# Kernel optimization log

Hardware: AMD Instinct MI355X
Metric: run time of the kernel (lower is better)

The kernel has to match this reference:

```python
import jax, jax.numpy as jnp
import numpy as np

ORDER = 5
LOOKAHEAD = 0
NDF = 96  # n_df_bins


def setup_inputs() -> dict:
    key = jax.random.key(0)
    k1, k2, k3 = jax.random.split(key, 3)
    spec = jax.random.normal(k1, (16, 1, 2000, 481, 2), dtype=jnp.float32)
    coefs = jax.random.normal(k2, (16, 2000, ORDER, NDF, 2), dtype=jnp.float32)
    alpha = jax.random.uniform(k3, (16, 2000, 1), dtype=jnp.float32)
    return {"spec": spec, "coefs": coefs, "alpha": alpha}


def reference(spec, coefs, alpha):
    # spec: [B, 1, T, F, 2]; coefs: [B, T, ORDER, NDF, 2]; alpha: [B, T, 1]
    B, _, T, F, _ = spec.shape
    x = spec[:, 0, :, :NDF, :]  # [B, T, NDF, 2]
    # pad time axis: (order - lookahead - 1) before, lookahead after
    xp = jnp.pad(x, ((0, 0), (ORDER - LOOKAHEAD - 1, LOOKAHEAD), (0, 0), (0, 0)))
    # overlapping time windows of length ORDER (loop over small fixed tap count)
    w = jnp.stack([xp[:, k:k + T] for k in range(ORDER)], axis=2)  # [B, T, ORDER, NDF, 2]
    # complex multiply-accumulate per tap, then sum over taps
    re = w[..., 0] * coefs[..., 0] - w[..., 1] * coefs[..., 1]
    im = w[..., 1] * coefs[..., 0] + w[..., 0] * coefs[..., 1]
    spec_f = jnp.stack((re, im), axis=-1).sum(axis=2)  # [B, T, NDF, 2]
    # alpha blend on the low df_bins, copy the rest unchanged
    a = alpha.reshape(B, 1, T, 1, 1)
    mixed = spec_f[:, None] * a + spec[..., :NDF, :] * (1.0 - a)
    return spec.at[..., :NDF, :].set(mixed)
```

## Files before the change

### kernel.cpp

```cpp
#include <hip/hip_runtime.h>

#define BB 16
#define TT 2000
#define FF 481
#define NDF_ 96
#define ORDER_ 5


__global__ __launch_bounds__(256) void df_op_kernel(
    const float* __restrict__ spec,
    const float* __restrict__ coefs,
    const float* __restrict__ alpha,
    float* __restrict__ out)
{
    const int bt = blockIdx.x;
    const int b  = bt / TT;
    const int t  = bt - b * TT;
    const int tid = threadIdx.x;

    const long row = (long)bt * (FF * 2);
    const float a = alpha[bt];
    const float oma = 1.0f - a;

    if (tid < NDF_) {
        const int f = tid;
        float acc_re = 0.0f, acc_im = 0.0f;
        const float2* cbase = (const float2*)(coefs + (long)bt * (ORDER_ * NDF_ * 2) + f * 2);
        #pragma unroll
        for (int k = 0; k < ORDER_; ++k) {
            const int tk = t - (ORDER_ - 1) + k;
            float2 x = make_float2(0.0f, 0.0f);
            if (tk >= 0) {
                x = *(const float2*)(spec + ((long)b * TT + tk) * (FF * 2) + f * 2);
            }
            const float2 c = cbase[k * NDF_];
            acc_re += x.x * c.x - x.y * c.y;
            acc_im += x.y * c.x + x.x * c.y;
        }
        const float2 s = *(const float2*)(spec + row + f * 2);
        float2 o;
        o.x = acc_re * a + s.x * oma;
        o.y = acc_im * a + s.y * oma;
        *(float2*)(out + row + f * 2) = o;
    }

    const float2* src = (const float2*)(spec + row + NDF_ * 2);
    float2*       dst = (float2*)(out + row + NDF_ * 2);
    for (int i = tid; i < (FF - NDF_); i += 256) {
        dst[i] = src[i];
    }
}

extern "C" void kernel_launch(void* const* d_in, const int* in_sizes, int n_in,
                              void* d_out, int out_size, void* d_ws, size_t ws_size,
                              hipStream_t stream) {
    const float* spec  = (const float*)d_in[0];
    const float* coefs = (const float*)d_in[1];
    const float* alpha = (const float*)d_in[2];
    float* out = (float*)d_out;

    dim3 grid(BB * TT);
    dim3 block(256);
    df_op_kernel<<<grid, block, 0, stream>>>(spec, coefs, alpha, out);
}
```

Measured before the change: 288.3 us.

## Split into bulk vectorized copy kernel plus batched DF compute kernel

The single per-row kernel is replaced by two launches. The first copies the whole spec tensor to the output with 16-byte nontemporal loads and stores. The second computes the deep-filter blend for the first 96 bins, processing 8 time rows per 768-thread block so no threads sit idle. This removes the poorly vectorized, partly idle per-row copy, but it writes the low 96 bins twice and adds a second launch.

```diff
diff --git a/kernel.cpp b/kernel.cpp
--- a/kernel.cpp
+++ b/kernel.cpp
@@ -5,50 +5,58 @@
 #define FF 481
 #define NDF_ 96
 #define ORDER_ 5
+#define ROW_F 962
+#define COEF_ROW_F 960
 
+typedef float floatx4 __attribute__((ext_vector_type(4)));
 
-__global__ __launch_bounds__(256) void df_op_kernel(
+__global__ __launch_bounds__(256) void copy_kernel(
+    const floatx4* __restrict__ src, floatx4* __restrict__ dst, int n4)
+{
+    int idx    = blockIdx.x * 256 + threadIdx.x;
+    int stride = gridDim.x * 256;
+    for (int i = idx; i < n4; i += stride) {
+        floatx4 v = __builtin_nontemporal_load(&src[i]);
+        __builtin_nontemporal_store(v, &dst[i]);
+    }
+}
+
+__global__ __launch_bounds__(768) void df_kernel(
     const float* __restrict__ spec,
     const float* __restrict__ coefs,
     const float* __restrict__ alpha,
     float* __restrict__ out)
 {
-    const int bt = blockIdx.x;
-    const int b  = bt / TT;
-    const int t  = bt - b * TT;
-    const int tid = threadIdx.x;
+    const int b  = blockIdx.x / 250;
+    const int t0 = (blockIdx.x - b * 250) * 8;
+    const int r  = threadIdx.x / 96;
+    const int f  = threadIdx.x - r * 96;
+    const int t  = t0 + r;
+    const int bt = b * TT + t;
 
-    const long row = (long)bt * (FF * 2);
-    const float a = alpha[bt];
+    const float a   = alpha[bt];
     const float oma = 1.0f - a;
 
-    if (tid < NDF_) {
-        const int f = tid;
-        float acc_re = 0.0f, acc_im = 0.0f;
-        const float2* cbase = (const float2*)(coefs + (long)bt * (ORDER_ * NDF_ * 2) + f * 2);
-        #pragma unroll
-        for (int k = 0; k < ORDER_; ++k) {
-            const int tk = t - (ORDER_ - 1) + k;
-            float2 x = make_float2(0.0f, 0.0f);
-            if (tk >= 0) {
-                x = *(const float2*)(spec + ((long)b * TT + tk) * (FF * 2) + f * 2);
-            }
-            const float2 c = cbase[k * NDF_];
-            acc_re += x.x * c.x - x.y * c.y;
-            acc_im += x.y * c.x + x.x * c.y;
+    float acc_re = 0.0f, acc_im = 0.0f;
+    const float2* cbase = (const float2*)(coefs + (long)bt * COEF_ROW_F + f * 2);
+    #pragma unroll
+    for (int k = 0; k < ORDER_; ++k) {
+        const int tk = t - (ORDER_ - 1) + k;
+        float2 x = make_float2(0.0f, 0.0f);
+        if (tk >= 0) {
+            x = *(const float2*)(spec + ((long)b * TT + tk) * ROW_F + f * 2);
         }
-        const float2 s = *(const float2*)(spec + row + f * 2);
-        float2 o;
-        o.x = acc_re * a + s.x * oma;
-        o.y = acc_im * a + s.y * oma;
-        *(float2*)(out + row + f * 2) = o;
+        const float2 c = cbase[k * NDF_];
+        acc_re += x.x * c.x - x.y * c.y;
+        acc_im += x.y * c.x + x.x * c.y;
     }
 
-    const float2* src = (const float2*)(spec + row + NDF_ * 2);
-    float2*       dst = (float2*)(out + row + NDF_ * 2);
-    for (int i = tid; i < (FF - NDF_); i += 256) {
-        dst[i] = src[i];
-    }
+    const long row = (long)bt * ROW_F;
+    const float2 s = *(const float2*)(spec + row + f * 2);
+    float2 o;
+    o.x = acc_re * a + s.x * oma;
+    o.y = acc_im * a + s.y * oma;
+    *(float2*)(out + row + f * 2) = o;
 }
 
 extern "C" void kernel_launch(void* const* d_in, const int* in_sizes, int n_in,
@@ -59,7 +67,8 @@
     const float* alpha = (const float*)d_in[2];
     float* out = (float*)d_out;
 
-    dim3 grid(BB * TT);
-    dim3 block(256);
-    df_op_kernel<<<grid, block, 0, stream>>>(spec, coefs, alpha, out);
+    const int n4 = (BB * TT * FF * 2) / 4;
+    copy_kernel<<<8192, 256, 0, stream>>>((const floatx4*)spec, (floatx4*)out, n4);
+
+    df_kernel<<<BB * 250, 768, 0, stream>>>(spec, coefs, alpha, out);
 }
```

Result: slower. 300.9 us (+4.4%).
